# Kernel tuning notes

Measured on AMD Instinct MI355X. Metric: run time of the kernel, lower is better.

The kernel has to match this reference:

```python
import jax, jax.numpy as jnp
import numpy as np

LEVELS = 4
ATOMS_PER_LEVEL = [8, 16, 32, 64]   # [8] doubled per level
TOTAL_ATOMS = sum(ATOMS_PER_LEVEL)  # 120
KS = [2, 4, 8, 16]
CONNECTIVITY = 4


def _connection_matrices():
    # For each level i (except last), a [A_next, A_prev] count matrix C where
    # C[idx, j] += 1 for idx in [(2j + t) % A_next for t in range(4)].
    mats = []
    for i in range(LEVELS - 1):
        a_prev, a_next = ATOMS_PER_LEVEL[i], ATOMS_PER_LEVEL[i + 1]
        C = np.zeros((a_next, a_prev), dtype=np.float32)
        for j in range(a_prev):
            for t in range(j * 2, CONNECTIVITY + j * 2):
                C[t % a_next, j] += 1.0
        mats.append(jnp.asarray(C))
    return mats

CONN_MATS = _connection_matrices()


def _topk_keep(x, k):
    # Keep top-k by |value| along channel dim (axis=1), zero elsewhere.
    xt = jnp.moveaxis(x, 1, -1)              # [B,H,W,C]
    B, H, W, C = xt.shape
    xf = xt.reshape(-1, C)                   # [N,C]
    _, idx = jax.lax.top_k(jnp.abs(xf), k)   # [N,k]
    rows = jnp.arange(xf.shape[0])[:, None]
    mask = jnp.zeros(xf.shape, dtype=bool).at[rows, idx].set(True)
    out = jnp.where(mask, xf, jnp.zeros((), xf.dtype))
    return jnp.moveaxis(out.reshape(B, H, W, C), -1, 1)


def setup_inputs() -> dict:
    key = jax.random.key(0)
    kx, kw, kb = jax.random.split(key, 3)
    x = jax.random.normal(kx, (8, 3, 256, 256), dtype=jnp.float32)
    w = jax.random.normal(kw, (TOTAL_ATOMS, 3, 3, 3), dtype=jnp.float32) * 0.1
    b = jax.random.normal(kb, (TOTAL_ATOMS,), dtype=jnp.float32) * 0.01
    return {"x": x, "w": w, "b": b}


def reference(x, w, b):
    # Dictionary conv: 3x3, stride 1, VALID padding -> [B, 120, H-2, W-2]
    all_act = jax.lax.conv_general_dilated(
        x, w, window_strides=(1, 1), padding='VALID',
        dimension_numbers=('NCHW', 'OIHW', 'NCHW')) + b[None, :, None, None]

    outs = []
    descending_mask = None
    idx = 0
    for i, n_atoms in enumerate(ATOMS_PER_LEVEL):
        act = all_act[:, idx:idx + n_atoms]  # [B, A_i, H', W']
        idx += n_atoms
        if descending_mask is not None:
            # OR-gate: sum parent masks into connected child channels, threshold.
            gating = jnp.einsum('np,bphw->bnhw', CONN_MATS[i - 1], descending_mask)
            act = act * (gating > 0).astype(act.dtype)
        selected = _topk_keep(act, KS[i])
        descending_mask = (selected != 0).astype(act.dtype)
        outs.append(selected)
    return jnp.concatenate(outs, axis=1)
```

## Files before the change

kernel.cpp:

```cpp
#include <hip/hip_runtime.h>
#include <stdint.h>

static constexpr int HIN = 256, WIN = 256, HO = 254, WOUT = 254, NB = 8;
static constexpr int PLANE = HO * WOUT;
static constexpr int PIX = NB * PLANE;

__device__ __forceinline__ uint64_t spread_pairs(uint64_t mask, int a_next) {
  uint64_t s = mask;
  s = (s | (s << 16)) & 0x0000FFFF0000FFFFull;
  s = (s | (s << 8))  & 0x00FF00FF00FF00FFull;
  s = (s | (s << 4))  & 0x0F0F0F0F0F0F0F0Full;
  s = (s | (s << 2))  & 0x3333333333333333ull;
  s = (s | (s << 1))  & 0x5555555555555555ull;
  uint64_t pair = s | (s << 1);
  uint64_t lim = (a_next >= 64) ? ~0ull : ((1ull << a_next) - 1ull);
  uint64_t rot = ((pair << 2) | (pair >> (a_next - 2))) & lim;
  return (pair | rot) & lim;
}

template<int K>
__device__ __forceinline__ void bsort_desc(uint32_t (&v)[K]) {
#pragma unroll
  for (int sz = 2; sz <= K; sz <<= 1) {
#pragma unroll
    for (int st = sz >> 1; st > 0; st >>= 1) {
#pragma unroll
      for (int i = 0; i < K; ++i) {
        int l = i ^ st;
        if (l > i) {
          uint32_t a = v[i], c = v[l];
          uint32_t mx = a > c ? a : c;
          uint32_t mn = a > c ? c : a;
          bool desc = ((i & sz) == 0);
          v[i] = desc ? mx : mn;
          v[l] = desc ? mn : mx;
        }
      }
    }
  }
}

template<int K>
__device__ __forceinline__ void bmerge_desc(uint32_t (&v)[K]) {
#pragma unroll
  for (int st = K >> 1; st > 0; st >>= 1) {
#pragma unroll
    for (int i = 0; i < K; ++i) {
      int l = i ^ st;
      if (l > i) {
        uint32_t a = v[i], c = v[l];
        v[i] = a > c ? a : c;
        v[l] = a > c ? c : a;
      }
    }
  }
}

template<int N, int K, bool GATE>
__device__ __forceinline__ uint64_t do_level(const float (&px)[27],
    const float* __restrict__ w, const float* __restrict__ b,
    int ch0, uint64_t allow, float* __restrict__ out, size_t out_base) {
  float act[N];
#pragma unroll
  for (int j = 0; j < N; ++j) {
    const float* wp = w + (size_t)(ch0 + j) * 27;
    float acc = 0.0f;
#pragma unroll
    for (int ky = 0; ky < 3; ++ky)
#pragma unroll
      for (int kx = 0; kx < 3; ++kx)
#pragma unroll
        for (int c = 0; c < 3; ++c) {
          int t = c * 9 + ky * 3 + kx;
          acc = __fmaf_rn(px[t], wp[t], acc);
        }
    acc = __fadd_rn(acc, b[ch0 + j]);
    if (GATE) acc = ((allow >> j) & 1ull) ? acc : 0.0f;
    act[j] = acc;
  }

  constexpr int G = N / K;
  uint32_t run[K];
#pragma unroll
  for (int i = 0; i < K; ++i)
    run[i] = __float_as_uint(act[i]) & 0x7fffffffu;
  bsort_desc<K>(run);

  uint32_t mb = 0;
#pragma unroll
  for (int g = 1; g < G; ++g) {
    uint32_t tmp[K];
#pragma unroll
    for (int i = 0; i < K; ++i)
      tmp[i] = __float_as_uint(act[g * K + i]) & 0x7fffffffu;
    bsort_desc<K>(tmp);
#pragma unroll
    for (int i = 0; i < K; ++i) {
      uint32_t c = tmp[K - 1 - i];
      run[i] = run[i] > c ? run[i] : c;
    }
    if (g < G - 1) {
      bmerge_desc<K>(run);
    } else {
      mb = run[0];
#pragma unroll
      for (int i = 1; i < K; ++i) mb = mb < run[i] ? mb : run[i];
    }
  }
  float m = __uint_as_float(mb);

  int base = 0;
#pragma unroll
  for (int j = 0; j < N; ++j) base += (fabsf(act[j]) > m) ? 1 : 0;
  int quota = K - base;

  uint64_t msk = 0;
#pragma unroll
  for (int j = 0; j < N; ++j) {
    float aj = fabsf(act[j]);
    bool eq = (aj == m);
    bool keep = (aj > m) || (eq && quota > 0);
    quota -= eq ? 1 : 0;
    float v = keep ? act[j] : 0.0f;
    out[out_base + (size_t)(ch0 + j) * PLANE] = v;
    msk |= (v != 0.0f) ? (1ull << j) : 0ull;
  }
  return msk;
}

__global__ __launch_bounds__(256, 4)
void hrtk_main(const float* __restrict__ x, const float* __restrict__ w,
               const float* __restrict__ b, float* __restrict__ out) {
  int p = blockIdx.x * blockDim.x + threadIdx.x;
  if (p >= PIX) return;
  int bi = p / PLANE;
  int r  = p % PLANE;
  int h  = r / WOUT;
  int wc = r % WOUT;

  float px[27];
  const float* xb = x + (size_t)bi * 3 * HIN * WIN;
#pragma unroll
  for (int c = 0; c < 3; ++c)
#pragma unroll
    for (int dy = 0; dy < 3; ++dy)
#pragma unroll
      for (int dx = 0; dx < 3; ++dx)
        px[c * 9 + dy * 3 + dx] =
            xb[c * HIN * WIN + (size_t)(h + dy) * WIN + (wc + dx)];

  size_t out_base = (size_t)bi * 120 * PLANE + (size_t)h * WOUT + wc;

  uint64_t m0 = do_level<8, 2, false>(px, w, b, 0, 0, out, out_base);
  uint64_t a1 = spread_pairs(m0, 16);
  uint64_t m1 = do_level<16, 4, true>(px, w, b, 8, a1, out, out_base);
  uint64_t a2 = spread_pairs(m1, 32);
  uint64_t m2 = do_level<32, 8, true>(px, w, b, 24, a2, out, out_base);
  uint64_t a3 = spread_pairs(m2, 64);
  (void)do_level<64, 16, true>(px, w, b, 56, a3, out, out_base);
}

extern "C" void kernel_launch(void* const* d_in, const int* in_sizes, int n_in,
                              void* d_out, int out_size, void* d_ws, size_t ws_size,
                              hipStream_t stream) {
  const float* x = (const float*)d_in[0];
  const float* w = (const float*)d_in[1];
  const float* b = (const float*)d_in[2];
  float* out = (float*)d_out;
  dim3 blk(256), grid((PIX + 255) / 256);
  hrtk_main<<<grid, blk, 0, stream>>>(x, w, b, out);
}
```

Before: 347.1 us.

## Split fused level pipeline into four per-level kernels passing gating masks through output

Replaces the single kernel that computed all four hierarchy levels per pixel with four kernels, one per level. The gating mask for each next level is stashed in the output channels that the next kernel later overwrites. Each kernel gets its own launch bounds, so the smaller levels can run with fewer registers and more waves. The quota computation now reads equal-count from the sorted network instead of rescanning, and output addressing uses 32-bit byte offsets. In exchange it adds three launches, reloads the input patches in every kernel, and adds extra global round-trips for the masks.

```diff
diff --git a/kernel.cpp b/kernel.cpp
--- a/kernel.cpp
+++ b/kernel.cpp
@@ -4,6 +4,7 @@
 static constexpr int HIN = 256, WIN = 256, HO = 254, WOUT = 254, NB = 8;
 static constexpr int PLANE = HO * WOUT;
 static constexpr int PIX = NB * PLANE;
+
 
 __device__ __forceinline__ uint64_t spread_pairs(uint64_t mask, int a_next) {
   uint64_t s = mask;
@@ -40,12 +41,11 @@
   }
 }
 
-template<int K>
-__device__ __forceinline__ void bmerge_desc(uint32_t (&v)[K]) {
-#pragma unroll
-  for (int st = K >> 1; st > 0; st >>= 1) {
-#pragma unroll
-    for (int i = 0; i < K; ++i) {
+__device__ __forceinline__ void bmerge16(uint32_t (&v)[16]) {
+#pragma unroll
+  for (int st = 8; st > 0; st >>= 1) {
+#pragma unroll
+    for (int i = 0; i < 16; ++i) {
       int l = i ^ st;
       if (l > i) {
         uint32_t a = v[i], c = v[l];
@@ -56,64 +56,43 @@
   }
 }
 
-template<int N, int K, bool GATE>
-__device__ __forceinline__ uint64_t do_level(const float (&px)[27],
-    const float* __restrict__ w, const float* __restrict__ b,
-    int ch0, uint64_t allow, float* __restrict__ out, size_t out_base) {
-  float act[N];
-#pragma unroll
-  for (int j = 0; j < N; ++j) {
-    const float* wp = w + (size_t)(ch0 + j) * 27;
-    float acc = 0.0f;
-#pragma unroll
-    for (int ky = 0; ky < 3; ++ky)
-#pragma unroll
-      for (int kx = 0; kx < 3; ++kx)
-#pragma unroll
-        for (int c = 0; c < 3; ++c) {
-          int t = c * 9 + ky * 3 + kx;
-          acc = __fmaf_rn(px[t], wp[t], acc);
-        }
-    acc = __fadd_rn(acc, b[ch0 + j]);
-    if (GATE) acc = ((allow >> j) & 1ull) ? acc : 0.0f;
-    act[j] = acc;
-  }
-
-  constexpr int G = N / K;
-  uint32_t run[K];
-#pragma unroll
-  for (int i = 0; i < K; ++i)
-    run[i] = __float_as_uint(act[i]) & 0x7fffffffu;
-  bsort_desc<K>(run);
-
-  uint32_t mb = 0;
-#pragma unroll
-  for (int g = 1; g < G; ++g) {
-    uint32_t tmp[K];
-#pragma unroll
-    for (int i = 0; i < K; ++i)
-      tmp[i] = __float_as_uint(act[g * K + i]) & 0x7fffffffu;
-    bsort_desc<K>(tmp);
-#pragma unroll
-    for (int i = 0; i < K; ++i) {
-      uint32_t c = tmp[K - 1 - i];
-      run[i] = run[i] > c ? run[i] : c;
-    }
-    if (g < G - 1) {
-      bmerge_desc<K>(run);
-    } else {
-      mb = run[0];
-#pragma unroll
-      for (int i = 1; i < K; ++i) mb = mb < run[i] ? mb : run[i];
-    }
-  }
-  float m = __uint_as_float(mb);
-
-  int base = 0;
-#pragma unroll
-  for (int j = 0; j < N; ++j) base += (fabsf(act[j]) > m) ? 1 : 0;
-  int quota = K - base;
-
+__device__ __forceinline__ void load_px(const float* __restrict__ x, int p,
+                                        float (&px)[27], uint32_t& tofs4) {
+  int bi = p / PLANE;
+  int r  = p % PLANE;
+  int h  = r / WOUT;
+  int wc = r % WOUT;
+  const float* xb = x + (size_t)bi * 3 * HIN * WIN;
+#pragma unroll
+  for (int c = 0; c < 3; ++c)
+#pragma unroll
+    for (int dy = 0; dy < 3; ++dy)
+#pragma unroll
+      for (int dx = 0; dx < 3; ++dx)
+        px[c * 9 + dy * 3 + dx] =
+            xb[c * HIN * WIN + (size_t)(h + dy) * WIN + (wc + dx)];
+  tofs4 = (uint32_t)(bi * 120 * PLANE + r) * 4u;
+}
+
+__device__ __forceinline__ float conv_atom(const float (&px)[27],
+                                           const float* __restrict__ wp,
+                                           float bias) {
+  float acc = 0.0f;
+#pragma unroll
+  for (int ky = 0; ky < 3; ++ky)
+#pragma unroll
+    for (int kx = 0; kx < 3; ++kx)
+#pragma unroll
+      for (int c = 0; c < 3; ++c) {
+        int t = c * 9 + ky * 3 + kx;
+        acc = __fmaf_rn(px[t], wp[t], acc);
+      }
+  return __fadd_rn(acc, bias);
+}
+
+template<int N>
+__device__ __forceinline__ uint64_t keep_store(const float (&act)[N], float m,
+    int quota, char* __restrict__ outB, uint32_t tofs4, int ch0) {
   uint64_t msk = 0;
 #pragma unroll
   for (int j = 0; j < N; ++j) {
@@ -122,42 +101,161 @@
     bool keep = (aj > m) || (eq && quota > 0);
     quota -= eq ? 1 : 0;
     float v = keep ? act[j] : 0.0f;
-    out[out_base + (size_t)(ch0 + j) * PLANE] = v;
+    *(float*)(outB + (size_t)(ch0 + j) * PLANE * 4 + tofs4) = v;
     msk |= (v != 0.0f) ? (1ull << j) : 0ull;
   }
   return msk;
 }
 
+__global__ __launch_bounds__(256, 8)
+void lvl0(const float* __restrict__ x, const float* __restrict__ w,
+          const float* __restrict__ b, float* __restrict__ out) {
+  int p = blockIdx.x * blockDim.x + threadIdx.x;
+  if (p >= PIX) return;
+  float px[27]; uint32_t tofs4;
+  load_px(x, p, px, tofs4);
+  char* outB = (char*)out;
+
+  float act[8];
+#pragma unroll
+  for (int j = 0; j < 8; ++j) act[j] = conv_atom(px, w + j * 27, b[j]);
+
+  uint32_t v[8];
+#pragma unroll
+  for (int i = 0; i < 8; ++i) v[i] = __float_as_uint(act[i]) & 0x7fffffffu;
+  bsort_desc<8>(v);
+  uint32_t mb = v[1];
+  float m = __uint_as_float(mb);
+  int base = 0;
+#pragma unroll
+  for (int j = 0; j < 8; ++j) base += (fabsf(act[j]) > m) ? 1 : 0;
+  int quota = 2 - base;
+
+  uint64_t msk = keep_store<8>(act, m, quota, outB, tofs4, 0);
+  uint32_t a1 = (uint32_t)spread_pairs(msk, 16);
+  *(uint32_t*)(outB + (size_t)8 * PLANE * 4 + tofs4) = a1;
+}
+
+__global__ __launch_bounds__(256, 6)
+void lvl1(const float* __restrict__ x, const float* __restrict__ w,
+          const float* __restrict__ b, float* __restrict__ out) {
+  int p = blockIdx.x * blockDim.x + threadIdx.x;
+  if (p >= PIX) return;
+  float px[27]; uint32_t tofs4;
+  load_px(x, p, px, tofs4);
+  char* outB = (char*)out;
+  uint32_t allow = *(const uint32_t*)(outB + (size_t)8 * PLANE * 4 + tofs4);
+
+  float act[16];
+#pragma unroll
+  for (int j = 0; j < 16; ++j) {
+    float a = conv_atom(px, w + (8 + j) * 27, b[8 + j]);
+    act[j] = ((allow >> j) & 1u) ? a : 0.0f;
+  }
+
+  uint32_t v[16];
+#pragma unroll
+  for (int i = 0; i < 16; ++i) v[i] = __float_as_uint(act[i]) & 0x7fffffffu;
+  bsort_desc<16>(v);
+  uint32_t mb = v[3];
+  float m = __uint_as_float(mb);
+  int quota = 0;
+#pragma unroll
+  for (int i = 0; i < 4; ++i) quota += (v[i] == mb) ? 1 : 0;
+
+  uint64_t msk = keep_store<16>(act, m, quota, outB, tofs4, 8);
+  uint32_t a2 = (uint32_t)spread_pairs(msk, 32);
+  *(uint32_t*)(outB + (size_t)24 * PLANE * 4 + tofs4) = a2;
+}
+
+__global__ __launch_bounds__(256, 5)
+void lvl2(const float* __restrict__ x, const float* __restrict__ w,
+          const float* __restrict__ b, float* __restrict__ out) {
+  int p = blockIdx.x * blockDim.x + threadIdx.x;
+  if (p >= PIX) return;
+  float px[27]; uint32_t tofs4;
+  load_px(x, p, px, tofs4);
+  char* outB = (char*)out;
+  uint32_t allow = *(const uint32_t*)(outB + (size_t)24 * PLANE * 4 + tofs4);
+
+  float act[32];
+#pragma unroll
+  for (int j = 0; j < 32; ++j) {
+    float a = conv_atom(px, w + (24 + j) * 27, b[24 + j]);
+    act[j] = ((allow >> j) & 1u) ? a : 0.0f;
+  }
+
+  uint32_t run[16], tmp[16];
+#pragma unroll
+  for (int i = 0; i < 16; ++i) run[i] = __float_as_uint(act[i]) & 0x7fffffffu;
+#pragma unroll
+  for (int i = 0; i < 16; ++i) tmp[i] = __float_as_uint(act[16 + i]) & 0x7fffffffu;
+  bsort_desc<16>(run);
+  bsort_desc<16>(tmp);
+#pragma unroll
+  for (int i = 0; i < 16; ++i) {
+    uint32_t c = tmp[15 - i];
+    run[i] = run[i] > c ? run[i] : c;
+  }
+  bmerge16(run);
+  uint32_t mb = run[7];
+  float m = __uint_as_float(mb);
+  int quota = 0;
+#pragma unroll
+  for (int i = 0; i < 8; ++i) quota += (run[i] == mb) ? 1 : 0;
+
+  uint64_t msk = keep_store<32>(act, m, quota, outB, tofs4, 24);
+  uint64_t a3 = spread_pairs(msk, 64);
+  *(uint32_t*)(outB + (size_t)56 * PLANE * 4 + tofs4) = (uint32_t)a3;
+  *(uint32_t*)(outB + (size_t)57 * PLANE * 4 + tofs4) = (uint32_t)(a3 >> 32);
+}
+
 __global__ __launch_bounds__(256, 4)
-void hrtk_main(const float* __restrict__ x, const float* __restrict__ w,
-               const float* __restrict__ b, float* __restrict__ out) {
-  int p = blockIdx.x * blockDim.x + threadIdx.x;
-  if (p >= PIX) return;
-  int bi = p / PLANE;
-  int r  = p % PLANE;
-  int h  = r / WOUT;
-  int wc = r % WOUT;
-
-  float px[27];
-  const float* xb = x + (size_t)bi * 3 * HIN * WIN;
-#pragma unroll
-  for (int c = 0; c < 3; ++c)
-#pragma unroll
-    for (int dy = 0; dy < 3; ++dy)
-#pragma unroll
-      for (int dx = 0; dx < 3; ++dx)
-        px[c * 9 + dy * 3 + dx] =
-            xb[c * HIN * WIN + (size_t)(h + dy) * WIN + (wc + dx)];
-
-  size_t out_base = (size_t)bi * 120 * PLANE + (size_t)h * WOUT + wc;
-
-  uint64_t m0 = do_level<8, 2, false>(px, w, b, 0, 0, out, out_base);
-  uint64_t a1 = spread_pairs(m0, 16);
-  uint64_t m1 = do_level<16, 4, true>(px, w, b, 8, a1, out, out_base);
-  uint64_t a2 = spread_pairs(m1, 32);
-  uint64_t m2 = do_level<32, 8, true>(px, w, b, 24, a2, out, out_base);
-  uint64_t a3 = spread_pairs(m2, 64);
-  (void)do_level<64, 16, true>(px, w, b, 56, a3, out, out_base);
+void lvl3(const float* __restrict__ x, const float* __restrict__ w,
+          const float* __restrict__ b, float* __restrict__ out) {
+  int p = blockIdx.x * blockDim.x + threadIdx.x;
+  if (p >= PIX) return;
+  float px[27]; uint32_t tofs4;
+  load_px(x, p, px, tofs4);
+  char* outB = (char*)out;
+  uint32_t lo = *(const uint32_t*)(outB + (size_t)56 * PLANE * 4 + tofs4);
+  uint32_t hi = *(const uint32_t*)(outB + (size_t)57 * PLANE * 4 + tofs4);
+  uint64_t allow = (uint64_t)lo | ((uint64_t)hi << 32);
+
+  float act[64];
+#pragma unroll
+  for (int j = 0; j < 64; ++j) {
+    float a = conv_atom(px, w + (56 + j) * 27, b[56 + j]);
+    act[j] = ((allow >> j) & 1ull) ? a : 0.0f;
+  }
+
+  uint32_t run[16];
+#pragma unroll
+  for (int i = 0; i < 16; ++i) run[i] = __float_as_uint(act[i]) & 0x7fffffffu;
+  bsort_desc<16>(run);
+#pragma unroll
+  for (int g = 1; g < 4; ++g) {
+    uint32_t tmp[16];
+#pragma unroll
+    for (int i = 0; i < 16; ++i)
+      tmp[i] = __float_as_uint(act[g * 16 + i]) & 0x7fffffffu;
+    bsort_desc<16>(tmp);
+#pragma unroll
+    for (int i = 0; i < 16; ++i) {
+      uint32_t c = tmp[15 - i];
+      run[i] = run[i] > c ? run[i] : c;
+    }
+    if (g < 3) bmerge16(run);
+  }
+  uint32_t mb = run[0];
+#pragma unroll
+  for (int i = 1; i < 16; ++i) mb = mb < run[i] ? mb : run[i];
+  float m = __uint_as_float(mb);
+  int quota = 0;
+#pragma unroll
+  for (int i = 0; i < 16; ++i) quota += (run[i] == mb) ? 1 : 0;
+
+  (void)keep_store<64>(act, m, quota, outB, tofs4, 56);
 }
 
 extern "C" void kernel_launch(void* const* d_in, const int* in_sizes, int n_in,
@@ -168,5 +266,8 @@
   const float* b = (const float*)d_in[2];
   float* out = (float*)d_out;
   dim3 blk(256), grid((PIX + 255) / 256);
-  hrtk_main<<<grid, blk, 0, stream>>>(x, w, b, out);
-}
+  lvl0<<<grid, blk, 0, stream>>>(x, w, b, out);
+  lvl1<<<grid, blk, 0, stream>>>(x, w, b, out);
+  lvl2<<<grid, blk, 0, stream>>>(x, w, b, out);
+  lvl3<<<grid, blk, 0, stream>>>(x, w, b, out);
+}
```

Result: slower. 362.6 us (+4.5%).

## Split into parallel conv kernel and separate top-k selection kernel through output buffer

Applied to the files above, without the earlier changes.

Splits the fused per-pixel kernel in two. The first kernel computes the conv for 8 channels per block across a 2D grid and writes the raw activations into the output buffer. The second kernel reads them back, applies gating and top-k per level, and writes the result in place, with a simplified quota computation taken from the sorted values. This raises parallelism and lowers register pressure in the conv stage, at the cost of an extra full write and read of the 120-channel output (about 250MB of traffic).

```diff
diff --git a/kernel.cpp b/kernel.cpp
--- a/kernel.cpp
+++ b/kernel.cpp
@@ -4,6 +4,7 @@
 static constexpr int HIN = 256, WIN = 256, HO = 254, WOUT = 254, NB = 8;
 static constexpr int PLANE = HO * WOUT;
 static constexpr int PIX = NB * PLANE;
+
 
 __device__ __forceinline__ uint64_t spread_pairs(uint64_t mask, int a_next) {
   uint64_t s = mask;
@@ -40,12 +41,11 @@
   }
 }
 
-template<int K>
-__device__ __forceinline__ void bmerge_desc(uint32_t (&v)[K]) {
-#pragma unroll
-  for (int st = K >> 1; st > 0; st >>= 1) {
-#pragma unroll
-    for (int i = 0; i < K; ++i) {
+__device__ __forceinline__ void bmerge16(uint32_t (&v)[16]) {
+#pragma unroll
+  for (int st = 8; st > 0; st >>= 1) {
+#pragma unroll
+    for (int i = 0; i < 16; ++i) {
       int l = i ^ st;
       if (l > i) {
         uint32_t a = v[i], c = v[l];
@@ -56,64 +56,25 @@
   }
 }
 
-template<int N, int K, bool GATE>
-__device__ __forceinline__ uint64_t do_level(const float (&px)[27],
-    const float* __restrict__ w, const float* __restrict__ b,
-    int ch0, uint64_t allow, float* __restrict__ out, size_t out_base) {
-  float act[N];
-#pragma unroll
-  for (int j = 0; j < N; ++j) {
-    const float* wp = w + (size_t)(ch0 + j) * 27;
-    float acc = 0.0f;
-#pragma unroll
-    for (int ky = 0; ky < 3; ++ky)
-#pragma unroll
-      for (int kx = 0; kx < 3; ++kx)
-#pragma unroll
-        for (int c = 0; c < 3; ++c) {
-          int t = c * 9 + ky * 3 + kx;
-          acc = __fmaf_rn(px[t], wp[t], acc);
-        }
-    acc = __fadd_rn(acc, b[ch0 + j]);
-    if (GATE) acc = ((allow >> j) & 1ull) ? acc : 0.0f;
-    act[j] = acc;
-  }
-
-  constexpr int G = N / K;
-  uint32_t run[K];
-#pragma unroll
-  for (int i = 0; i < K; ++i)
-    run[i] = __float_as_uint(act[i]) & 0x7fffffffu;
-  bsort_desc<K>(run);
-
-  uint32_t mb = 0;
-#pragma unroll
-  for (int g = 1; g < G; ++g) {
-    uint32_t tmp[K];
-#pragma unroll
-    for (int i = 0; i < K; ++i)
-      tmp[i] = __float_as_uint(act[g * K + i]) & 0x7fffffffu;
-    bsort_desc<K>(tmp);
-#pragma unroll
-    for (int i = 0; i < K; ++i) {
-      uint32_t c = tmp[K - 1 - i];
-      run[i] = run[i] > c ? run[i] : c;
-    }
-    if (g < G - 1) {
-      bmerge_desc<K>(run);
-    } else {
-      mb = run[0];
-#pragma unroll
-      for (int i = 1; i < K; ++i) mb = mb < run[i] ? mb : run[i];
-    }
-  }
-  float m = __uint_as_float(mb);
-
-  int base = 0;
-#pragma unroll
-  for (int j = 0; j < N; ++j) base += (fabsf(act[j]) > m) ? 1 : 0;
-  int quota = K - base;
-
+__device__ __forceinline__ float conv_atom(const float (&px)[27],
+                                           const float* __restrict__ wp,
+                                           float bias) {
+  float acc = 0.0f;
+#pragma unroll
+  for (int ky = 0; ky < 3; ++ky)
+#pragma unroll
+    for (int kx = 0; kx < 3; ++kx)
+#pragma unroll
+      for (int c = 0; c < 3; ++c) {
+        int t = c * 9 + ky * 3 + kx;
+        acc = __fmaf_rn(px[t], wp[t], acc);
+      }
+  return __fadd_rn(acc, bias);
+}
+
+template<int N>
+__device__ __forceinline__ uint64_t keep_store(const float (&act)[N], float m,
+    int quota, char* __restrict__ outB, uint32_t tofs4, int ch0) {
   uint64_t msk = 0;
 #pragma unroll
   for (int j = 0; j < N; ++j) {
@@ -122,42 +83,154 @@
     bool keep = (aj > m) || (eq && quota > 0);
     quota -= eq ? 1 : 0;
     float v = keep ? act[j] : 0.0f;
-    out[out_base + (size_t)(ch0 + j) * PLANE] = v;
+    *(float*)(outB + (size_t)(ch0 + j) * PLANE * 4 + tofs4) = v;
     msk |= (v != 0.0f) ? (1ull << j) : 0ull;
   }
   return msk;
 }
 
+__global__ __launch_bounds__(256, 8)
+void conv_phase(const float* __restrict__ x, const float* __restrict__ w,
+                const float* __restrict__ b, float* __restrict__ out) {
+  int p = blockIdx.x * blockDim.x + threadIdx.x;
+  if (p >= PIX) return;
+  int ch0 = blockIdx.y * 8;
+  int bi = p / PLANE;
+  int r  = p % PLANE;
+  int h  = r / WOUT;
+  int wc = r % WOUT;
+
+  float px[27];
+  const float* xb = x + (size_t)bi * 3 * HIN * WIN;
+#pragma unroll
+  for (int c = 0; c < 3; ++c)
+#pragma unroll
+    for (int dy = 0; dy < 3; ++dy)
+#pragma unroll
+      for (int dx = 0; dx < 3; ++dx)
+        px[c * 9 + dy * 3 + dx] =
+            xb[c * HIN * WIN + (size_t)(h + dy) * WIN + (wc + dx)];
+
+  uint32_t tofs4 = (uint32_t)(bi * 120 * PLANE + r) * 4u;
+  char* outB = (char*)out;
+#pragma unroll
+  for (int j = 0; j < 8; ++j) {
+    float a = conv_atom(px, w + (size_t)(ch0 + j) * 27, b[ch0 + j]);
+    *(float*)(outB + (size_t)(ch0 + j) * PLANE * 4 + tofs4) = a;
+  }
+}
+
 __global__ __launch_bounds__(256, 4)
-void hrtk_main(const float* __restrict__ x, const float* __restrict__ w,
-               const float* __restrict__ b, float* __restrict__ out) {
+void select_phase(float* __restrict__ out) {
   int p = blockIdx.x * blockDim.x + threadIdx.x;
   if (p >= PIX) return;
   int bi = p / PLANE;
   int r  = p % PLANE;
-  int h  = r / WOUT;
-  int wc = r % WOUT;
-
-  float px[27];
-  const float* xb = x + (size_t)bi * 3 * HIN * WIN;
-#pragma unroll
-  for (int c = 0; c < 3; ++c)
-#pragma unroll
-    for (int dy = 0; dy < 3; ++dy)
-#pragma unroll
-      for (int dx = 0; dx < 3; ++dx)
-        px[c * 9 + dy * 3 + dx] =
-            xb[c * HIN * WIN + (size_t)(h + dy) * WIN + (wc + dx)];
-
-  size_t out_base = (size_t)bi * 120 * PLANE + (size_t)h * WOUT + wc;
-
-  uint64_t m0 = do_level<8, 2, false>(px, w, b, 0, 0, out, out_base);
-  uint64_t a1 = spread_pairs(m0, 16);
-  uint64_t m1 = do_level<16, 4, true>(px, w, b, 8, a1, out, out_base);
-  uint64_t a2 = spread_pairs(m1, 32);
-  uint64_t m2 = do_level<32, 8, true>(px, w, b, 24, a2, out, out_base);
-  uint64_t a3 = spread_pairs(m2, 64);
-  (void)do_level<64, 16, true>(px, w, b, 56, a3, out, out_base);
+  uint32_t tofs4 = (uint32_t)(bi * 120 * PLANE + r) * 4u;
+  char* outB = (char*)out;
+
+  float act0[8], act1[16], act2[32];
+#pragma unroll
+  for (int j = 0; j < 8; ++j)
+    act0[j] = *(const float*)(outB + (size_t)(0 + j) * PLANE * 4 + tofs4);
+#pragma unroll
+  for (int j = 0; j < 16; ++j)
+    act1[j] = *(const float*)(outB + (size_t)(8 + j) * PLANE * 4 + tofs4);
+#pragma unroll
+  for (int j = 0; j < 32; ++j)
+    act2[j] = *(const float*)(outB + (size_t)(24 + j) * PLANE * 4 + tofs4);
+
+  uint32_t v0[8];
+#pragma unroll
+  for (int i = 0; i < 8; ++i) v0[i] = __float_as_uint(act0[i]) & 0x7fffffffu;
+  bsort_desc<8>(v0);
+  uint32_t mb0 = v0[1];
+  float m0 = __uint_as_float(mb0);
+  int base0 = 0;
+#pragma unroll
+  for (int j = 0; j < 8; ++j) base0 += (fabsf(act0[j]) > m0) ? 1 : 0;
+  uint64_t msk0 = keep_store<8>(act0, m0, 2 - base0, outB, tofs4, 0);
+  uint32_t allow1 = (uint32_t)spread_pairs(msk0, 16);
+
+#pragma unroll
+  for (int j = 0; j < 16; ++j)
+    act1[j] = ((allow1 >> j) & 1u) ? act1[j] : 0.0f;
+  uint32_t v1[16];
+#pragma unroll
+  for (int i = 0; i < 16; ++i) v1[i] = __float_as_uint(act1[i]) & 0x7fffffffu;
+  bsort_desc<16>(v1);
+  uint32_t mb1 = v1[3];
+  float m1 = __uint_as_float(mb1);
+  int q1 = 0;
+#pragma unroll
+  for (int i = 0; i < 4; ++i) q1 += (v1[i] == mb1) ? 1 : 0;
+  uint64_t msk1 = keep_store<16>(act1, m1, q1, outB, tofs4, 8);
+  uint32_t allow2 = (uint32_t)spread_pairs(msk1, 32);
+
+#pragma unroll
+  for (int j = 0; j < 32; ++j)
+    act2[j] = ((allow2 >> j) & 1u) ? act2[j] : 0.0f;
+  {
+    uint32_t run[16], tmp[16];
+#pragma unroll
+    for (int i = 0; i < 16; ++i)
+      run[i] = __float_as_uint(act2[i]) & 0x7fffffffu;
+#pragma unroll
+    for (int i = 0; i < 16; ++i)
+      tmp[i] = __float_as_uint(act2[16 + i]) & 0x7fffffffu;
+    bsort_desc<16>(run);
+    bsort_desc<16>(tmp);
+#pragma unroll
+    for (int i = 0; i < 16; ++i) {
+      uint32_t c = tmp[15 - i];
+      run[i] = run[i] > c ? run[i] : c;
+    }
+    bmerge16(run);
+    uint32_t mb2 = run[7];
+    float m2 = __uint_as_float(mb2);
+    int q2 = 0;
+#pragma unroll
+    for (int i = 0; i < 8; ++i) q2 += (run[i] == mb2) ? 1 : 0;
+    uint64_t msk2 = keep_store<32>(act2, m2, q2, outB, tofs4, 24);
+    uint64_t allow3 = spread_pairs(msk2, 64);
+
+    float act3[64];
+#pragma unroll
+    for (int j = 0; j < 64; ++j)
+      act3[j] = *(const float*)(outB + (size_t)(56 + j) * PLANE * 4 + tofs4);
+#pragma unroll
+    for (int j = 0; j < 64; ++j)
+      act3[j] = ((allow3 >> j) & 1ull) ? act3[j] : 0.0f;
+
+    uint32_t r3[16];
+#pragma unroll
+    for (int i = 0; i < 16; ++i)
+      r3[i] = __float_as_uint(act3[i]) & 0x7fffffffu;
+    bsort_desc<16>(r3);
+#pragma unroll
+    for (int g = 1; g < 4; ++g) {
+      uint32_t t3[16];
+#pragma unroll
+      for (int i = 0; i < 16; ++i)
+        t3[i] = __float_as_uint(act3[g * 16 + i]) & 0x7fffffffu;
+      bsort_desc<16>(t3);
+#pragma unroll
+      for (int i = 0; i < 16; ++i) {
+        uint32_t c = t3[15 - i];
+        r3[i] = r3[i] > c ? r3[i] : c;
+      }
+      if (g < 3) bmerge16(r3);
+    }
+    uint32_t mb3 = r3[0];
+#pragma unroll
+    for (int i = 1; i < 16; ++i) mb3 = mb3 < r3[i] ? mb3 : r3[i];
+    float m3 = __uint_as_float(mb3);
+    int q3 = 0;
+#pragma unroll
+    for (int i = 0; i < 16; ++i) q3 += (r3[i] == mb3) ? 1 : 0;
+
+    (void)keep_store<64>(act3, m3, q3, outB, tofs4, 56);
+  }
 }
 
 extern "C" void kernel_launch(void* const* d_in, const int* in_sizes, int n_in,
@@ -167,6 +240,10 @@
   const float* w = (const float*)d_in[1];
   const float* b = (const float*)d_in[2];
   float* out = (float*)d_out;
-  dim3 blk(256), grid((PIX + 255) / 256);
-  hrtk_main<<<grid, blk, 0, stream>>>(x, w, b, out);
-}
+
+  dim3 blk(256);
+  dim3 g1((PIX + 255) / 256, 15);
+  dim3 g2((PIX + 255) / 256);
+  conv_phase<<<g1, blk, 0, stream>>>(x, w, b, out);
+  select_phase<<<g2, blk, 0, stream>>>(out);
+}
```

Result: slower. 557.7 us (+60.7%).
